# Kernel tuning notes

Hardware: AMD Instinct MI355X
Metric: run time of the kernel (lower is better)

The kernel has to match this reference:

```python
import jax, jax.numpy as jnp
import numpy as np

B, S, DIN, DOUT = 8, 2048, 512, 512

def setup_inputs() -> dict:
    key = jax.random.key(0)
    ks = jax.random.split(key, 9)
    s = 1.0 / np.sqrt(DIN)  # torch Linear default init scale
    return {
        "Q": jax.random.normal(ks[0], (B, S, DIN), jnp.float32),
        "K": jax.random.normal(ks[1], (B, S, DIN), jnp.float32),
        "V": jax.random.normal(ks[2], (B, S, DIN), jnp.float32),
        "Wq": jax.random.uniform(ks[3], (DIN, DOUT), jnp.float32, -s, s),
        "bq": jax.random.uniform(ks[4], (DOUT,), jnp.float32, -s, s),
        "Wk": jax.random.uniform(ks[5], (DIN, DOUT), jnp.float32, -s, s),
        "bk": jax.random.uniform(ks[6], (DOUT,), jnp.float32, -s, s),
        "Wv": jax.random.uniform(ks[7], (DIN, DOUT), jnp.float32, -s, s),
        "bv": jax.random.uniform(ks[8], (DOUT,), jnp.float32, -s, s),
    }

def reference(Q, K, V, Wq, bq, Wk, bk, Wv, bv):
    q = Q @ Wq + bq  # [B,S,D]
    k = K @ Wk + bk
    v = V @ Wv + bv
    # Unscaled attention, exactly as in the torch module
    attn = jnp.einsum('bqd,bkd->bqk', q, k)  # [B,S,S]
    attn_prob = jax.nn.softmax(attn, axis=-1)
    return jnp.einsum('bqk,bkd->bqd', attn_prob, v)
```

## Files before the change

### kernel.cpp

```cpp
#include <hip/hip_runtime.h>
#include <hip/hip_bf16.h>
#include <hip/hip_fp16.h>

#define B_ 8
#define S_ 2048
#define D_ 512

typedef _Float16 f16x8 __attribute__((ext_vector_type(8)));
typedef float f32x4 __attribute__((ext_vector_type(4)));

__global__ void wconv_kernel(const float* __restrict__ Wq,
                             const float* __restrict__ Wk,
                             const float* __restrict__ Wv,
                             _Float16* __restrict__ w_ws) {
    int idx = blockIdx.x * 256 + threadIdx.x;
    int which = blockIdx.y;
    const float* W = (which == 0) ? Wq : (which == 1) ? Wk : Wv;
    int n = idx >> 9;
    int k = idx & 511;
    w_ws[(size_t)which * D_ * D_ + (size_t)n * D_ + k] = (_Float16)W[(size_t)k * D_ + n];
}

__launch_bounds__(256)
__global__ void proj_kernel(const float* __restrict__ Q,
                            const float* __restrict__ K,
                            const float* __restrict__ V,
                            const _Float16* __restrict__ w_ws,
                            const float* __restrict__ bq,
                            const float* __restrict__ bk,
                            const float* __restrict__ bv,
                            _Float16* __restrict__ q_ws,
                            _Float16* __restrict__ k_ws,
                            _Float16* __restrict__ v_ws) {
    const int which = blockIdx.z;
    const float* X    = (which == 0) ? Q  : (which == 1) ? K  : V;
    const float* bias = (which == 0) ? bq : (which == 1) ? bk : bv;
    const _Float16* Wt = w_ws + (size_t)which * D_ * D_;

    const int Mb = blockIdx.x * 128;
    const int Nb = blockIdx.y * 128;
    const int t = threadIdx.x;
    const int w = t >> 6;
    const int l = t & 63;
    const int lr = l & 15;
    const int lk = (l >> 4) * 8;
    const int lq = (l >> 4) * 4;

    f32x4 acc[2][8] = {};

    for (int k0 = 0; k0 < D_; k0 += 32) {
        f16x8 a[2], bfr[8];
#pragma unroll
        for (int mi = 0; mi < 2; mi++) {
            int row = Mb + w * 32 + mi * 16 + lr;
            const float* p = X + (size_t)row * D_ + k0 + lk;
            float xa[8];
            *(float4*)&xa[0] = *(const float4*)p;
            *(float4*)&xa[4] = *(const float4*)(p + 4);
#pragma unroll
            for (int j = 0; j < 8; j++) a[mi][j] = (_Float16)xa[j];
        }
#pragma unroll
        for (int ni = 0; ni < 8; ni++) {
            int col = Nb + ni * 16 + lr;
            bfr[ni] = *(const f16x8*)(Wt + (size_t)col * D_ + k0 + lk);
        }
#pragma unroll
        for (int mi = 0; mi < 2; mi++)
#pragma unroll
            for (int ni = 0; ni < 8; ni++)
                acc[mi][ni] = __builtin_amdgcn_mfma_f32_16x16x32_f16(a[mi], bfr[ni], acc[mi][ni], 0, 0, 0);
    }

#pragma unroll
    for (int ni = 0; ni < 8; ni++) {
        int col = Nb + ni * 16 + lr;
        float bn = bias[col];
#pragma unroll
        for (int mi = 0; mi < 2; mi++) {
#pragma unroll
            for (int j = 0; j < 4; j++) {
                int row = Mb + w * 32 + mi * 16 + lq + j;
                float vv = acc[mi][ni][j] + bn;
                if (which == 0) {
                    q_ws[(size_t)row * D_ + col] = (_Float16)vv;
                } else if (which == 1) {
                    k_ws[(size_t)row * D_ + col] = (_Float16)vv;
                } else {
                    int bb = row >> 11, s = row & 2047;
                    v_ws[((size_t)bb * D_ + col) * S_ + s] = (_Float16)vv;
                }
            }
        }
    }
}

__launch_bounds__(512)
__global__ void attn_kernel(const _Float16* __restrict__ q_ws,
                            const _Float16* __restrict__ k_ws,
                            const _Float16* __restrict__ v_ws,
                            float* __restrict__ out) {
    __shared__ float    S_lds[64][132];
    __shared__ _Float16 P_lds[64][136];
    __shared__ float    m_lds[64];
    __shared__ float    l_lds[64];
    __shared__ float    alpha_lds[64];

    const int bid = blockIdx.x;
    const int b  = bid & 7;
    const int qb = (bid >> 3) * 64;

    const int t = threadIdx.x;
    const int w = t >> 6;
    const int l = t & 63;
    const int qg = w >> 2;
    const int kc = w & 3;
    const int lr = l & 15;
    const int lk = (l >> 4) * 8;
    const int lq = (l >> 4) * 4;

    const _Float16* qp = q_ws + (size_t)b * S_ * D_;
    const _Float16* kp = k_ws + (size_t)b * S_ * D_;
    const _Float16* vp = v_ws + (size_t)b * D_ * S_;

    if (t < 64) { m_lds[t] = -INFINITY; l_lds[t] = 0.f; }

    f32x4 oacc[2][8] = {};
    __syncthreads();

    for (int kv0 = 0; kv0 < S_; kv0 += 128) {
        f32x4 sacc[2][2] = {};
        for (int d0 = 0; d0 < D_; d0 += 32) {
            f16x8 aq[2], bk2[2];
#pragma unroll
            for (int mi = 0; mi < 2; mi++)
                aq[mi] = *(const f16x8*)(qp + (size_t)(qb + qg * 32 + mi * 16 + lr) * D_ + d0 + lk);
#pragma unroll
            for (int ni = 0; ni < 2; ni++)
                bk2[ni] = *(const f16x8*)(kp + (size_t)(kv0 + kc * 32 + ni * 16 + lr) * D_ + d0 + lk);
#pragma unroll
            for (int mi = 0; mi < 2; mi++)
#pragma unroll
                for (int ni = 0; ni < 2; ni++)
                    sacc[mi][ni] = __builtin_amdgcn_mfma_f32_16x16x32_f16(aq[mi], bk2[ni], sacc[mi][ni], 0, 0, 0);
        }
#pragma unroll
        for (int mi = 0; mi < 2; mi++)
#pragma unroll
            for (int ni = 0; ni < 2; ni++)
#pragma unroll
                for (int j = 0; j < 4; j++)
                    S_lds[qg * 32 + mi * 16 + lq + j][kc * 32 + ni * 16 + lr] = sacc[mi][ni][j];
        __syncthreads();

        {
            const int r = t >> 3;
            const int cs = (t & 7) * 16;
            float sv[16];
#pragma unroll
            for (int c4 = 0; c4 < 4; c4++)
                *(float4*)&sv[c4 * 4] = *(const float4*)&S_lds[r][cs + c4 * 4];
            float mx = sv[0];
#pragma unroll
            for (int c = 1; c < 16; c++) mx = fmaxf(mx, sv[c]);
            mx = fmaxf(mx, __shfl_xor(mx, 1));
            mx = fmaxf(mx, __shfl_xor(mx, 2));
            mx = fmaxf(mx, __shfl_xor(mx, 4));
            float m_old = m_lds[r];
            float m_new = fmaxf(m_old, mx);
            float ps = 0.f;
            f16x8 p0, p1;
#pragma unroll
            for (int c = 0; c < 8; c++) {
                float p = __expf(sv[c] - m_new);
                ps += p;
                p0[c] = (_Float16)p;
            }
#pragma unroll
            for (int c = 0; c < 8; c++) {
                float p = __expf(sv[c + 8] - m_new);
                ps += p;
                p1[c] = (_Float16)p;
            }
            *(f16x8*)&P_lds[r][cs]     = p0;
            *(f16x8*)&P_lds[r][cs + 8] = p1;
            ps += __shfl_xor(ps, 1);
            ps += __shfl_xor(ps, 2);
            ps += __shfl_xor(ps, 4);
            if ((t & 7) == 0) {
                float al = __expf(m_old - m_new);
                alpha_lds[r] = al;
                l_lds[r] = l_lds[r] * al + ps;
                m_lds[r] = m_new;
            }
        }
        __syncthreads();

#pragma unroll
        for (int mi = 0; mi < 2; mi++)
#pragma unroll
            for (int j = 0; j < 4; j++) {
                float al = alpha_lds[qg * 32 + mi * 16 + lq + j];
#pragma unroll
                for (int ni = 0; ni < 8; ni++) oacc[mi][ni][j] *= al;
            }

        for (int ks = 0; ks < 4; ks++) {
            f16x8 pa[2], vb[8];
#pragma unroll
            for (int mi = 0; mi < 2; mi++)
                pa[mi] = *(const f16x8*)&P_lds[qg * 32 + mi * 16 + lr][ks * 32 + lk];
#pragma unroll
            for (int ni = 0; ni < 8; ni++)
                vb[ni] = *(const f16x8*)(vp + (size_t)(kc * 128 + ni * 16 + lr) * S_ + kv0 + ks * 32 + lk);
#pragma unroll
            for (int mi = 0; mi < 2; mi++)
#pragma unroll
                for (int ni = 0; ni < 8; ni++)
                    oacc[mi][ni] = __builtin_amdgcn_mfma_f32_16x16x32_f16(pa[mi], vb[ni], oacc[mi][ni], 0, 0, 0);
        }
        __syncthreads();
    }

#pragma unroll
    for (int mi = 0; mi < 2; mi++)
#pragma unroll
        for (int j = 0; j < 4; j++) {
            int row = qg * 32 + mi * 16 + lq + j;
            float rl = 1.f / l_lds[row];
#pragma unroll
            for (int ni = 0; ni < 8; ni++) {
                int col = kc * 128 + ni * 16 + lr;
                out[((size_t)b * S_ + qb + row) * D_ + col] = oacc[mi][ni][j] * rl;
            }
        }
}

extern "C" void kernel_launch(void* const* d_in, const int* in_sizes, int n_in,
                              void* d_out, int out_size, void* d_ws, size_t ws_size,
                              hipStream_t stream) {
    const float* Q  = (const float*)d_in[0];
    const float* K  = (const float*)d_in[1];
    const float* V  = (const float*)d_in[2];
    const float* Wq = (const float*)d_in[3];
    const float* bq = (const float*)d_in[4];
    const float* Wk = (const float*)d_in[5];
    const float* bk = (const float*)d_in[6];
    const float* Wv = (const float*)d_in[7];
    const float* bv = (const float*)d_in[8];
    float* out = (float*)d_out;

    char* ws = (char*)d_ws;
    _Float16* w_ws = (_Float16*)ws;
    _Float16* q_ws = (_Float16*)(ws + 3ull * 512 * 512 * 2);
    _Float16* k_ws = q_ws + 8ull * 2048 * 512;
    _Float16* v_ws = k_ws + 8ull * 2048 * 512;

    wconv_kernel<<<dim3(1024, 3), 256, 0, stream>>>(Wq, Wk, Wv, w_ws);
    proj_kernel<<<dim3(128, 4, 3), 256, 0, stream>>>(Q, K, V, w_ws, bq, bk, bv, q_ws, k_ws, v_ws);
    attn_kernel<<<dim3(256), 512, 0, stream>>>(q_ws, k_ws, v_ws, out);
}
```

Measured before the change: 556.2 us.

## Stage projection tiles in LDS and widen attention blocks to 1024 threads

The projection GEMM now copies swizzled X and W tiles into shared memory with global_load_lds, instead of having each wave read global memory directly. Its grid is also reordered so blocks that share an M tile run next to each other. The attention kernel moves to 16 waves per block, a 256-wide KV tile and a 64-column output slice per wave, and drops the trailing barrier in each iteration. The aim is more latency hiding and fewer loop iterations and barriers, at the cost of more LDS use (about 100KB) and more register pressure at 1024 threads per block.

```diff
diff --git a/kernel.cpp b/kernel.cpp
--- a/kernel.cpp
+++ b/kernel.cpp
@@ -8,6 +8,12 @@
 
 typedef _Float16 f16x8 __attribute__((ext_vector_type(8)));
 typedef float f32x4 __attribute__((ext_vector_type(4)));
+
+__device__ __forceinline__ void gload16(const void* g, void* l) {
+    __builtin_amdgcn_global_load_lds(
+        (const __attribute__((address_space(1))) void*)g,
+        (__attribute__((address_space(3))) void*)l, 16, 0, 0);
+}
 
 __global__ void wconv_kernel(const float* __restrict__ Wq,
                              const float* __restrict__ Wk,
@@ -32,13 +38,16 @@
                             _Float16* __restrict__ q_ws,
                             _Float16* __restrict__ k_ws,
                             _Float16* __restrict__ v_ws) {
+    __shared__ __align__(16) float    As[128 * 32];
+    __shared__ __align__(16) _Float16 Bs[128 * 32];
+
     const int which = blockIdx.z;
     const float* X    = (which == 0) ? Q  : (which == 1) ? K  : V;
     const float* bias = (which == 0) ? bq : (which == 1) ? bk : bv;
     const _Float16* Wt = w_ws + (size_t)which * D_ * D_;
 
-    const int Mb = blockIdx.x * 128;
-    const int Nb = blockIdx.y * 128;
+    const int Nb = blockIdx.x * 128;
+    const int Mb = blockIdx.y * 128;
     const int t = threadIdx.x;
     const int w = t >> 6;
     const int l = t & 63;
@@ -49,27 +58,49 @@
     f32x4 acc[2][8] = {};
 
     for (int k0 = 0; k0 < D_; k0 += 32) {
-        f16x8 a[2], bfr[8];
+        {
+            int c = t;
+#pragma unroll
+            for (int i = 0; i < 4; i++, c += 256) {
+                int row = c >> 3, p = c & 7;
+                gload16(X + (size_t)(Mb + row) * D_ + k0 + ((p ^ (row & 7)) << 2),
+                        As + c * 4);
+            }
+        }
+        {
+            int c = t;
+#pragma unroll
+            for (int i = 0; i < 2; i++, c += 256) {
+                int col = c >> 2, p = c & 3;
+                gload16(Wt + (size_t)(Nb + col) * D_ + k0 + ((p ^ (col & 3)) << 3),
+                        Bs + c * 8);
+            }
+        }
+        __syncthreads();
+
+        f16x8 a[2], b[8];
 #pragma unroll
         for (int mi = 0; mi < 2; mi++) {
-            int row = Mb + w * 32 + mi * 16 + lr;
-            const float* p = X + (size_t)row * D_ + k0 + lk;
-            float xa[8];
-            *(float4*)&xa[0] = *(const float4*)p;
-            *(float4*)&xa[4] = *(const float4*)(p + 4);
-#pragma unroll
-            for (int j = 0; j < 8; j++) a[mi][j] = (_Float16)xa[j];
+            int row = w * 32 + mi * 16 + lr;
+            int s0 = lk >> 2;
+            const float* base = As + row * 32;
+            f32x4 a0 = *(const f32x4*)(base + ((s0 ^ (row & 7)) << 2));
+            f32x4 a1 = *(const f32x4*)(base + (((s0 + 1) ^ (row & 7)) << 2));
+#pragma unroll
+            for (int j = 0; j < 4; j++) { a[mi][j] = (_Float16)a0[j]; a[mi][4 + j] = (_Float16)a1[j]; }
         }
 #pragma unroll
         for (int ni = 0; ni < 8; ni++) {
-            int col = Nb + ni * 16 + lr;
-            bfr[ni] = *(const f16x8*)(Wt + (size_t)col * D_ + k0 + lk);
+            int col = ni * 16 + lr;
+            int s = lk >> 3;
+            b[ni] = *(const f16x8*)(Bs + col * 32 + ((s ^ (col & 3)) << 3));
         }
 #pragma unroll
         for (int mi = 0; mi < 2; mi++)
 #pragma unroll
             for (int ni = 0; ni < 8; ni++)
-                acc[mi][ni] = __builtin_amdgcn_mfma_f32_16x16x32_f16(a[mi], bfr[ni], acc[mi][ni], 0, 0, 0);
+                acc[mi][ni] = __builtin_amdgcn_mfma_f32_16x16x32_f16(a[mi], b[ni], acc[mi][ni], 0, 0, 0);
+        __syncthreads();
     }
 
 #pragma unroll
@@ -95,13 +126,13 @@
     }
 }
 
-__launch_bounds__(512)
+__launch_bounds__(1024)
 __global__ void attn_kernel(const _Float16* __restrict__ q_ws,
                             const _Float16* __restrict__ k_ws,
                             const _Float16* __restrict__ v_ws,
                             float* __restrict__ out) {
-    __shared__ float    S_lds[64][132];
-    __shared__ _Float16 P_lds[64][136];
+    __shared__ float    S_lds[64][260];
+    __shared__ _Float16 P_lds[64][264];
     __shared__ float    m_lds[64];
     __shared__ float    l_lds[64];
     __shared__ float    alpha_lds[64];
@@ -113,8 +144,8 @@
     const int t = threadIdx.x;
     const int w = t >> 6;
     const int l = t & 63;
-    const int qg = w >> 2;
-    const int kc = w & 3;
+    const int qg = w >> 3;
+    const int kc = w & 7;
     const int lr = l & 15;
     const int lk = (l >> 4) * 8;
     const int lq = (l >> 4) * 4;
@@ -125,10 +156,10 @@
 
     if (t < 64) { m_lds[t] = -INFINITY; l_lds[t] = 0.f; }
 
-    f32x4 oacc[2][8] = {};
+    f32x4 oacc[2][4] = {};
     __syncthreads();
 
-    for (int kv0 = 0; kv0 < S_; kv0 += 128) {
+    for (int kv0 = 0; kv0 < S_; kv0 += 256) {
         f32x4 sacc[2][2] = {};
         for (int d0 = 0; d0 < D_; d0 += 32) {
             f16x8 aq[2], bk2[2];
@@ -154,8 +185,8 @@
         __syncthreads();
 
         {
-            const int r = t >> 3;
-            const int cs = (t & 7) * 16;
+            const int r = t >> 4;
+            const int cs = (t & 15) * 16;
             float sv[16];
 #pragma unroll
             for (int c4 = 0; c4 < 4; c4++)
@@ -166,6 +197,7 @@
             mx = fmaxf(mx, __shfl_xor(mx, 1));
             mx = fmaxf(mx, __shfl_xor(mx, 2));
             mx = fmaxf(mx, __shfl_xor(mx, 4));
+            mx = fmaxf(mx, __shfl_xor(mx, 8));
             float m_old = m_lds[r];
             float m_new = fmaxf(m_old, mx);
             float ps = 0.f;
@@ -187,7 +219,8 @@
             ps += __shfl_xor(ps, 1);
             ps += __shfl_xor(ps, 2);
             ps += __shfl_xor(ps, 4);
-            if ((t & 7) == 0) {
+            ps += __shfl_xor(ps, 8);
+            if ((t & 15) == 0) {
                 float al = __expf(m_old - m_new);
                 alpha_lds[r] = al;
                 l_lds[r] = l_lds[r] * al + ps;
@@ -202,24 +235,23 @@
             for (int j = 0; j < 4; j++) {
                 float al = alpha_lds[qg * 32 + mi * 16 + lq + j];
 #pragma unroll
-                for (int ni = 0; ni < 8; ni++) oacc[mi][ni][j] *= al;
-            }
-
-        for (int ks = 0; ks < 4; ks++) {
-            f16x8 pa[2], vb[8];
+                for (int ni = 0; ni < 4; ni++) oacc[mi][ni][j] *= al;
+            }
+
+        for (int ks = 0; ks < 8; ks++) {
+            f16x8 pa[2], vb[4];
 #pragma unroll
             for (int mi = 0; mi < 2; mi++)
                 pa[mi] = *(const f16x8*)&P_lds[qg * 32 + mi * 16 + lr][ks * 32 + lk];
 #pragma unroll
-            for (int ni = 0; ni < 8; ni++)
-                vb[ni] = *(const f16x8*)(vp + (size_t)(kc * 128 + ni * 16 + lr) * S_ + kv0 + ks * 32 + lk);
-#pragma unroll
-            for (int mi = 0; mi < 2; mi++)
-#pragma unroll
-                for (int ni = 0; ni < 8; ni++)
+            for (int ni = 0; ni < 4; ni++)
+                vb[ni] = *(const f16x8*)(vp + (size_t)(kc * 64 + ni * 16 + lr) * S_ + kv0 + ks * 32 + lk);
+#pragma unroll
+            for (int mi = 0; mi < 2; mi++)
+#pragma unroll
+                for (int ni = 0; ni < 4; ni++)
                     oacc[mi][ni] = __builtin_amdgcn_mfma_f32_16x16x32_f16(pa[mi], vb[ni], oacc[mi][ni], 0, 0, 0);
         }
-        __syncthreads();
     }
 
 #pragma unroll
@@ -229,8 +261,8 @@
             int row = qg * 32 + mi * 16 + lq + j;
             float rl = 1.f / l_lds[row];
 #pragma unroll
-            for (int ni = 0; ni < 8; ni++) {
-                int col = kc * 128 + ni * 16 + lr;
+            for (int ni = 0; ni < 4; ni++) {
+                int col = kc * 64 + ni * 16 + lr;
                 out[((size_t)b * S_ + qb + row) * D_ + col] = oacc[mi][ni][j] * rl;
             }
         }
@@ -257,6 +289,6 @@
     _Float16* v_ws = k_ws + 8ull * 2048 * 512;
 
     wconv_kernel<<<dim3(1024, 3), 256, 0, stream>>>(Wq, Wk, Wv, w_ws);
-    proj_kernel<<<dim3(128, 4, 3), 256, 0, stream>>>(Q, K, V, w_ws, bq, bk, bv, q_ws, k_ws, v_ws);
-    attn_kernel<<<dim3(256), 512, 0, stream>>>(q_ws, k_ws, v_ws, out);
-}
+    proj_kernel<<<dim3(4, 128, 3), 256, 0, stream>>>(Q, K, V, w_ws, bq, bk, bv, q_ws, k_ws, v_ws);
+    attn_kernel<<<dim3(256), 1024, 0, stream>>>(q_ws, k_ws, v_ws, out);
+}
```

Result: no change. 556.8 us (+0.1%).
